# Performance work log

Measured on AMD Instinct MI355X. Metric: run time of the kernel, lower is better.

Reference implementation:

```python
import jax, jax.numpy as jnp
import numpy as np

N_NODES = 50000
N_EDGES = 640000
D_FEAT = 128
NUM_RELS = 8
EPS = 0.0  # init_eps=0, learn_eps=False -> constant buffer


def setup_inputs() -> dict:
    key = jax.random.key(0)
    k_feat, k_w, k_et, k_src, k_dst = jax.random.split(key, 5)
    feat = jax.random.normal(k_feat, (N_NODES, D_FEAT), dtype=jnp.float32)
    # TypedLinear weight: one [in_feat, out_feat] matrix per relation
    W = jax.random.normal(k_w, (NUM_RELS, D_FEAT, D_FEAT), dtype=jnp.float32) * 0.05
    etypes = jax.random.randint(k_et, (N_EDGES,), 0, NUM_RELS, dtype=jnp.int32)
    src = jax.random.randint(k_src, (N_EDGES,), 0, N_NODES, dtype=jnp.int32)
    dst = jax.random.randint(k_dst, (N_EDGES,), 0, N_NODES, dtype=jnp.int32)
    return {"feat": feat, "W": W, "etypes": etypes, "src": src, "dst": dst}


def reference(feat, W, etypes, src, dst):
    # feat: [N, d]; W: [R, d, d]; etypes/src/dst: [E]
    n_nodes = feat.shape[0]
    num_rels = W.shape[0]
    x = feat[src]  # gather source features, [E, d]
    # TypedLinear: m_e = x_e @ W[etype_e]. Loop over the small fixed relation
    # set (grouped-GEMM form) instead of materializing [E, d, d] weights.
    m = jnp.zeros_like(x)
    for r in range(num_rels):
        mask = (etypes == r)[:, None]
        m = m + jnp.where(mask, x, 0.0) @ W[r]
    # sum aggregation over destination nodes (update_all with fn.sum)
    neigh = jax.ops.segment_sum(m, dst, num_segments=n_nodes)  # [N, d]
    # GIN update: (1 + eps) * h + sum of messages; apply_func/activation are None
    return (1.0 + EPS) * feat + neigh
```

## Files before the change

kernel.cpp:

```cpp
#include <hip/hip_runtime.h>
#include <hip/hip_bf16.h>
#include <stdint.h>

#define D 128

using bf16x8 = __attribute__((ext_vector_type(8))) short;
using f32x4  = __attribute__((ext_vector_type(4))) float;

__device__ __forceinline__ unsigned short f2bf(float f) {
    unsigned u = __float_as_uint(f);
    u = (u + 0x7fffu + ((u >> 16) & 1u)) >> 16;
    return (unsigned short)u;
}
__device__ __forceinline__ float bf2f(unsigned short h) {
    return __uint_as_float(((unsigned)h) << 16);
}

__device__ __forceinline__ bf16x8 cvt8(float4 a, float4 b) {
    union { bf16x8 v; __hip_bfloat162 h[4]; } u;
    u.h[0] = __float22bfloat162_rn(make_float2(a.x, a.y));
    u.h[1] = __float22bfloat162_rn(make_float2(a.z, a.w));
    u.h[2] = __float22bfloat162_rn(make_float2(b.x, b.y));
    u.h[3] = __float22bfloat162_rn(make_float2(b.z, b.w));
    return u.v;
}

__device__ __forceinline__ uint4 pack2(f32x4 x, f32x4 y) {
    union { uint4 u; __hip_bfloat162 h[4]; } o;
    o.h[0] = __float22bfloat162_rn(make_float2(x[0], x[1]));
    o.h[1] = __float22bfloat162_rn(make_float2(x[2], x[3]));
    o.h[2] = __float22bfloat162_rn(make_float2(y[0], y[1]));
    o.h[3] = __float22bfloat162_rn(make_float2(y[2], y[3]));
    return o.u;
}

__global__ __launch_bounds__(256) void prep_wt_kernel(
    const float* __restrict__ W, unsigned short* __restrict__ Wt, int total)
{
    int idx = blockIdx.x * 256 + threadIdx.x;
    if (idx >= total) return;
    int r = idx >> 14;
    int rem = idx & 16383;
    int k = rem >> 7, c = rem & 127;
    Wt[(r << 14) + (c << 7) + k] = f2bf(W[idx]);
}

__global__ __launch_bounds__(256) void fused_transform_count_kernel(
    const float* __restrict__ feat, const unsigned short* __restrict__ Wt,
    unsigned short* __restrict__ H,
    const int* __restrict__ dst, int* __restrict__ deg, int* __restrict__ ord,
    int N, int NBX, int tBlocks, int E)
{
    __shared__ __align__(16) unsigned short sW[128 * 128];
    const int b = blockIdx.x;

    if (b >= tBlocks) {
        int e = (b - tBlocks) * 256 + threadIdx.x;
        if (e < E) ord[e] = atomicAdd(&deg[dst[e]], 1);
        return;
    }

    const int rel = b / NBX;
    const int bx  = b - rel * NBX;
    const int tid  = threadIdx.x;
    const int wave = tid >> 6, lane = tid & 63;
    const int q    = lane >> 4, mlo = lane & 15;

    {
        const ulonglong2* wsrc = (const ulonglong2*)(Wt + ((size_t)rel << 14));
        #pragma unroll
        for (int i = 0; i < 8; ++i) {
            int idx = tid + 256 * i;
            int row = idx >> 4, ch = idx & 15;
            ulonglong2 v = wsrc[idx];
            *(ulonglong2*)&sW[row * 128 + ((ch ^ (row & 15)) * 8)] = v;
        }
    }

    const int nb = bx * 128 + wave * 32;
    bf16x8 bfr[2][4];
    int nodeg[2];
    #pragma unroll
    for (int g = 0; g < 2; ++g) {
        int node = nb + g * 16 + mlo;
        nodeg[g] = node;
        int ld = node < N ? node : N - 1;
        const float* fp = feat + (size_t)ld * D + q * 8;
        #pragma unroll
        for (int ks = 0; ks < 4; ++ks)
            bfr[g][ks] = cvt8(*(const float4*)(fp + ks * 32), *(const float4*)(fp + ks * 32 + 4));
    }
    __syncthreads();

    const size_t Hb = (size_t)rel * N * D;
    unsigned short* hp0 = H + Hb + (size_t)nodeg[0] * D + q * 8;
    unsigned short* hp1 = H + Hb + (size_t)nodeg[1] * D + q * 8;

    #pragma unroll
    for (int j = 0; j < 4; ++j) {
        bf16x8 af0[4], af1[4];
        const int row0 = (2 * j) * 16 + mlo, row1 = row0 + 16;
        #pragma unroll
        for (int ks = 0; ks < 4; ++ks) {
            af0[ks] = *(const bf16x8*)&sW[row0 * 128 + (((ks * 4 + q) ^ mlo) * 8)];
            af1[ks] = *(const bf16x8*)&sW[row1 * 128 + (((ks * 4 + q) ^ mlo) * 8)];
        }
        #pragma unroll
        for (int g = 0; g < 2; ++g) {
            f32x4 a = {0.f,0.f,0.f,0.f}, c = {0.f,0.f,0.f,0.f};
            #pragma unroll
            for (int ks = 0; ks < 4; ++ks) {
                a = __builtin_amdgcn_mfma_f32_16x16x32_bf16(af0[ks], bfr[g][ks], a, 0, 0, 0);
                c = __builtin_amdgcn_mfma_f32_16x16x32_bf16(af1[ks], bfr[g][ks], c, 0, 0, 0);
            }
            if (nodeg[g] < N)
                *(uint4*)((g ? hp1 : hp0) + j * 32) = pack2(a, c);
        }
    }
}

__global__ __launch_bounds__(256) void k_blocksum(
    const int* __restrict__ deg, int* __restrict__ part, int N)
{
    int t = threadIdx.x, i = blockIdx.x * 256 + t;
    int v = (i < N) ? deg[i] : 0;
    #pragma unroll
    for (int o = 32; o > 0; o >>= 1) v += __shfl_down(v, o, 64);
    __shared__ int ws_[4];
    if ((t & 63) == 0) ws_[t >> 6] = v;
    __syncthreads();
    if (t == 0) part[blockIdx.x] = ws_[0] + ws_[1] + ws_[2] + ws_[3];
}

__global__ __launch_bounds__(256) void k_scanpart(int* part, int nb)
{
    __shared__ int s[256];
    int t = threadIdx.x;
    int v = (t < nb) ? part[t] : 0;
    s[t] = v;
    #pragma unroll
    for (int o = 1; o < 256; o <<= 1) {
        __syncthreads();
        int x = (t >= o) ? s[t - o] : 0;
        __syncthreads();
        s[t] += x;
    }
    if (t < nb) part[t] = s[t] - v;
}

__global__ __launch_bounds__(256) void k_scanfinal(
    const int* __restrict__ deg, const int* __restrict__ part,
    int* __restrict__ off, int N, int E)
{
    __shared__ int s[256];
    int t = threadIdx.x, i = blockIdx.x * 256 + t;
    int v = (i < N) ? deg[i] : 0;
    s[t] = v;
    #pragma unroll
    for (int o = 1; o < 256; o <<= 1) {
        __syncthreads();
        int x = (t >= o) ? s[t - o] : 0;
        __syncthreads();
        s[t] += x;
    }
    if (i < N) off[i] = part[blockIdx.x] + s[t] - v;
    if (i == 0) off[N] = E;
}

__global__ __launch_bounds__(256) void k_fill(
    const int* __restrict__ dst, const int* __restrict__ et,
    const int* __restrict__ src, const int* __restrict__ off,
    const int* __restrict__ ord, unsigned int* __restrict__ sorted, int E, int N)
{
    int e = blockIdx.x * 256 + threadIdx.x;
    if (e >= E) return;
    unsigned key = ((unsigned)et[e] * (unsigned)N + (unsigned)src[e]) << 8;
    sorted[off[dst[e]] + ord[e]] = key;
}

__global__ __launch_bounds__(256) void k_gather4(
    const char* __restrict__ Hc, const unsigned int* __restrict__ sorted,
    const int* __restrict__ off, const float* __restrict__ feat,
    float* __restrict__ out, int N)
{
    int n = blockIdx.x * 4 + (threadIdx.x >> 6);
    if (n >= N) return;
    int lane = threadIdx.x & 63;

    const int jj = lane >> 4, qq = (lane >> 2) & 3, pp = lane & 3;
    const int f = 16 * jj + 8 * (pp >> 1) + 2 * qq + (pp & 1);

    float2 acc = ((const float2*)feat)[(size_t)n * 64 + f];

    int j0 = __builtin_amdgcn_readfirstlane(off[n]);
    int j1 = __builtin_amdgcn_readfirstlane(off[n + 1]);
    int deg = j1 - j0;
    if (deg > 0) {
        unsigned ep = sorted[j0 + (lane < deg ? lane : deg - 1)];
        int capped = deg < 64 ? deg : 64;
        for (int done = 0; done < capped; done += 16) {
            unsigned a[16];
            #pragma unroll
            for (int u = 0; u < 16; ++u) {
                int idx = done + u; idx = idx < capped ? idx : capped - 1;
                unsigned p = __shfl(ep, idx);
                a[u] = *(const unsigned*)(Hc + p + lane * 4);
            }
            #pragma unroll
            for (int u = 0; u < 16; ++u) {
                bool v = (done + u) < capped;
                acc.x += v ? bf2f((unsigned short)(a[u] & 0xffffu)) : 0.f;
                acc.y += v ? bf2f((unsigned short)(a[u] >> 16)) : 0.f;
            }
        }
        for (int j = j0 + 64; j < j1; ++j) {
            unsigned p = sorted[j];
            unsigned a0 = *(const unsigned*)(Hc + p + lane * 4);
            acc.x += bf2f((unsigned short)(a0 & 0xffffu));
            acc.y += bf2f((unsigned short)(a0 >> 16));
        }
    }
    ((float2*)out)[(size_t)n * 64 + f] = acc;
}

__global__ __launch_bounds__(256) void init_kernel(
    const float* __restrict__ feat, float* __restrict__ out, int n4)
{
    int i = blockIdx.x * 256 + threadIdx.x;
    if (i < n4) ((float4*)out)[i] = ((const float4*)feat)[i];
}

__global__ __launch_bounds__(128) void edge_matvec_kernel(
    const float* __restrict__ feat, const float* __restrict__ W,
    const int* __restrict__ et, const int* __restrict__ src,
    const int* __restrict__ dst, float* __restrict__ out, int E)
{
    __shared__ float xs[D];
    int e = blockIdx.x;
    int c = threadIdx.x;
    int s = src[e], r = et[e], d = dst[e];
    xs[c] = feat[(size_t)s * D + c];
    __syncthreads();
    const float* Wr = W + (size_t)r * D * D;
    float acc = 0.f;
    #pragma unroll 8
    for (int k = 0; k < D; ++k) acc += xs[k] * Wr[(size_t)k * D + c];
    atomicAdd(out + (size_t)d * D + c, acc);
}

static inline size_t al256(size_t x) { return (x + 255) & ~(size_t)255; }

extern "C" void kernel_launch(void* const* d_in, const int* in_sizes, int n_in,
                              void* d_out, int out_size, void* d_ws, size_t ws_size,
                              hipStream_t stream) {
    const float* feat = (const float*)d_in[0];
    const float* W    = (const float*)d_in[1];
    const int*   et   = (const int*)d_in[2];
    const int*   src  = (const int*)d_in[3];
    const int*   dst  = (const int*)d_in[4];
    float* out = (float*)d_out;

    const int N = in_sizes[0] / D;
    const int R = in_sizes[1] / (D * D);
    const int E = in_sizes[2];

    size_t hB   = al256((size_t)R * N * D * sizeof(unsigned short));
    size_t wtB  = al256((size_t)R * D * D * sizeof(unsigned short));
    size_t offB = al256((size_t)(N + 1) * sizeof(int));
    size_t degB = al256((size_t)N * sizeof(int));
    size_t ordB = al256((size_t)E * sizeof(int));
    size_t parB = al256(1024 * sizeof(int));
    size_t srtB = al256((size_t)E * sizeof(unsigned int));
    size_t need = hB + wtB + offB + degB + ordB + parB + srtB;

    const int nbScan = (N + 255) / 256;
    const bool packable = (nbScan <= 256) &&
                          ((size_t)R * (size_t)N * 256ull <= 0xFFFFFFFFull);

    if (ws_size >= need && packable) {
        char* p = (char*)d_ws;
        unsigned short* H      = (unsigned short*)p;           p += hB;
        unsigned short* Wt     = (unsigned short*)p;           p += wtB;
        int*            off    = (int*)p;                      p += offB;
        int*            deg    = (int*)p;                      p += degB;
        int*            ord    = (int*)p;                      p += ordB;
        int*            part   = (int*)p;                      p += parB;
        unsigned int*   sorted = (unsigned int*)p;

        int wtTotal = R * D * D;
        int cntBlocks = (E + 255) / 256;

        hipMemsetAsync(deg, 0, (size_t)N * sizeof(int), stream);
        prep_wt_kernel<<<(wtTotal + 255) / 256, 256, 0, stream>>>(W, Wt, wtTotal);

        int NBX = (N + 127) / 128;
        int tBlocks = NBX * R;
        fused_transform_count_kernel<<<tBlocks + cntBlocks, 256, 0, stream>>>(
            feat, Wt, H, dst, deg, ord, N, NBX, tBlocks, E);

        k_blocksum<<<nbScan, 256, 0, stream>>>(deg, part, N);
        k_scanpart<<<1, 256, 0, stream>>>(part, nbScan);
        k_scanfinal<<<nbScan, 256, 0, stream>>>(deg, part, off, N, E);
        k_fill<<<cntBlocks, 256, 0, stream>>>(dst, et, src, off, ord, sorted, E, N);

        k_gather4<<<(N + 3) / 4, 256, 0, stream>>>((const char*)H, sorted, off, feat, out, N);
    } else {
        int n4 = (N * D) / 4;
        init_kernel<<<(n4 + 255) / 256, 256, 0, stream>>>(feat, out, n4);
        edge_matvec_kernel<<<E, 128, 0, stream>>>(feat, W, et, src, dst, out, E);
    }
}
```

Baseline: 201.8 us.

## Pre-convert features to bf16, interleave count blocks, widen gather loads

Adds a prep kernel that converts feat to bf16 once, so each of the 8 per-relation transform blocks reads half the bytes instead of re-reading fp32 features. Count blocks are spread evenly among transform blocks rather than appended at the end, so the atomic degree counting overlaps with the MFMA work. The gather kernel now has each half-wave handle a different edge with 8-byte loads and combines the halves with a cross-lane shuffle, which doubles the bytes per load instruction. This costs an extra bf16 feature buffer and an extra pass over feat.

```diff
diff --git a/kernel.cpp b/kernel.cpp
--- a/kernel.cpp
+++ b/kernel.cpp
@@ -34,34 +34,52 @@
     return o.u;
 }
 
-__global__ __launch_bounds__(256) void prep_wt_kernel(
-    const float* __restrict__ W, unsigned short* __restrict__ Wt, int total)
-{
-    int idx = blockIdx.x * 256 + threadIdx.x;
-    if (idx >= total) return;
-    int r = idx >> 14;
-    int rem = idx & 16383;
-    int k = rem >> 7, c = rem & 127;
-    Wt[(r << 14) + (c << 7) + k] = f2bf(W[idx]);
-}
-
-__global__ __launch_bounds__(256) void fused_transform_count_kernel(
-    const float* __restrict__ feat, const unsigned short* __restrict__ Wt,
+__global__ __launch_bounds__(256) void prep2_kernel(
+    const float* __restrict__ feat, unsigned short* __restrict__ featb,
+    const float* __restrict__ W, unsigned short* __restrict__ Wt,
+    int fcTotal , int wtTotal)
+{
+    int fcBlocks = (fcTotal + 255) >> 8;
+    int b = blockIdx.x;
+    if (b < fcBlocks) {
+        int i = b * 256 + threadIdx.x;
+        if (i < fcTotal) {
+            const float4* p = (const float4*)feat + (size_t)i * 2;
+            *(bf16x8*)(featb + (size_t)i * 8) = cvt8(p[0], p[1]);
+        }
+    } else {
+        int idx = (b - fcBlocks) * 256 + threadIdx.x;
+        if (idx < wtTotal) {
+            int r = idx >> 14;
+            int rem = idx & 16383;
+            int k = rem >> 7, c = rem & 127;
+            Wt[(r << 14) + (c << 7) + k] = f2bf(W[idx]);
+        }
+    }
+}
+
+__global__ __launch_bounds__(256) void fused2_kernel(
+    const unsigned short* __restrict__ featb, const unsigned short* __restrict__ Wt,
     unsigned short* __restrict__ H,
     const int* __restrict__ dst, int* __restrict__ deg, int* __restrict__ ord,
-    int N, int NBX, int tBlocks, int E)
+    int N, int NBX, int tBlocks, int cntBlocks, int E)
 {
     __shared__ __align__(16) unsigned short sW[128 * 128];
     const int b = blockIdx.x;
-
-    if (b >= tBlocks) {
-        int e = (b - tBlocks) * 256 + threadIdx.x;
+    const long long total = (long long)tBlocks + cntBlocks;
+
+    long long cb = ((long long)b * cntBlocks) / total;
+    bool isCount = (((long long)(b + 1) * cntBlocks) / total) > cb;
+
+    if (isCount) {
+        int e = (int)cb * 256 + threadIdx.x;
         if (e < E) ord[e] = atomicAdd(&deg[dst[e]], 1);
         return;
     }
 
-    const int rel = b / NBX;
-    const int bx  = b - rel * NBX;
+    const int tIdx = b - (int)cb;
+    const int rel = tIdx / NBX;
+    const int bx  = tIdx - rel * NBX;
     const int tid  = threadIdx.x;
     const int wave = tid >> 6, lane = tid & 63;
     const int q    = lane >> 4, mlo = lane & 15;
@@ -85,10 +103,10 @@
         int node = nb + g * 16 + mlo;
         nodeg[g] = node;
         int ld = node < N ? node : N - 1;
-        const float* fp = feat + (size_t)ld * D + q * 8;
+        const unsigned short* fp = featb + (size_t)ld * D + q * 8;
         #pragma unroll
         for (int ks = 0; ks < 4; ++ks)
-            bfr[g][ks] = cvt8(*(const float4*)(fp + ks * 32), *(const float4*)(fp + ks * 32 + 4));
+            bfr[g][ks] = *(const bf16x8*)(fp + ks * 32);
     }
     __syncthreads();
 
@@ -178,7 +196,7 @@
     sorted[off[dst[e]] + ord[e]] = key;
 }
 
-__global__ __launch_bounds__(256) void k_gather4(
+__global__ __launch_bounds__(256) void k_gather5(
     const char* __restrict__ Hc, const unsigned int* __restrict__ sorted,
     const int* __restrict__ off, const float* __restrict__ feat,
     float* __restrict__ out, int N)
@@ -186,41 +204,57 @@
     int n = blockIdx.x * 4 + (threadIdx.x >> 6);
     if (n >= N) return;
     int lane = threadIdx.x & 63;
-
-    const int jj = lane >> 4, qq = (lane >> 2) & 3, pp = lane & 3;
-    const int f = 16 * jj + 8 * (pp >> 1) + 2 * qq + (pp & 1);
-
-    float2 acc = ((const float2*)feat)[(size_t)n * 64 + f];
+    int h = lane >> 5, l5 = lane & 31;
+
+    float2 acc0 = {0.f, 0.f}, acc1 = {0.f, 0.f};
 
     int j0 = __builtin_amdgcn_readfirstlane(off[n]);
     int j1 = __builtin_amdgcn_readfirstlane(off[n + 1]);
     int deg = j1 - j0;
     if (deg > 0) {
+        int capped = deg < 64 ? deg : 64;
         unsigned ep = sorted[j0 + (lane < deg ? lane : deg - 1)];
-        int capped = deg < 64 ? deg : 64;
-        for (int done = 0; done < capped; done += 16) {
-            unsigned a[16];
+        for (int done = 0; done < capped; done += 32) {
+            unsigned long long a[16];
             #pragma unroll
             for (int u = 0; u < 16; ++u) {
-                int idx = done + u; idx = idx < capped ? idx : capped - 1;
-                unsigned p = __shfl(ep, idx);
-                a[u] = *(const unsigned*)(Hc + p + lane * 4);
+                int eidx = done + 2 * u + h;
+                int cl = eidx < capped ? eidx : capped - 1;
+                unsigned p = __shfl(ep, cl);
+                a[u] = *(const unsigned long long*)(Hc + p + l5 * 8);
             }
             #pragma unroll
             for (int u = 0; u < 16; ++u) {
-                bool v = (done + u) < capped;
-                acc.x += v ? bf2f((unsigned short)(a[u] & 0xffffu)) : 0.f;
-                acc.y += v ? bf2f((unsigned short)(a[u] >> 16)) : 0.f;
+                bool v = (done + 2 * u + h) < capped;
+                unsigned lo = (unsigned)a[u], hi = (unsigned)(a[u] >> 32);
+                acc0.x += v ? bf2f((unsigned short)(lo & 0xffffu)) : 0.f;
+                acc0.y += v ? bf2f((unsigned short)(lo >> 16)) : 0.f;
+                acc1.x += v ? bf2f((unsigned short)(hi & 0xffffu)) : 0.f;
+                acc1.y += v ? bf2f((unsigned short)(hi >> 16)) : 0.f;
             }
         }
-        for (int j = j0 + 64; j < j1; ++j) {
+        for (int j = j0 + 64 + h; j < j1; j += 2) {
             unsigned p = sorted[j];
-            unsigned a0 = *(const unsigned*)(Hc + p + lane * 4);
-            acc.x += bf2f((unsigned short)(a0 & 0xffffu));
-            acc.y += bf2f((unsigned short)(a0 >> 16));
-        }
-    }
-    ((float2*)out)[(size_t)n * 64 + f] = acc;
+            unsigned long long a0 = *(const unsigned long long*)(Hc + p + l5 * 8);
+            unsigned lo = (unsigned)a0, hi = (unsigned)(a0 >> 32);
+            acc0.x += bf2f((unsigned short)(lo & 0xffffu));
+            acc0.y += bf2f((unsigned short)(lo >> 16));
+            acc1.x += bf2f((unsigned short)(hi & 0xffffu));
+            acc1.y += bf2f((unsigned short)(hi >> 16));
+        }
+    }
+    acc0.x += __shfl(acc0.x, lane ^ 32);
+    acc0.y += __shfl(acc0.y, lane ^ 32);
+    acc1.x += __shfl(acc1.x, lane ^ 32);
+    acc1.y += __shfl(acc1.y, lane ^ 32);
+    if (h == 0) {
+        int f4 = 8 * (l5 >> 3) + 4 * (l5 & 1) + ((l5 >> 1) & 3);
+        float4 fv = ((const float4*)feat)[(size_t)n * 32 + f4];
+        float4 o;
+        o.x = fv.x + acc0.x; o.y = fv.y + acc0.y;
+        o.z = fv.z + acc1.x; o.w = fv.w + acc1.y;
+        ((float4*)out)[(size_t)n * 32 + f4] = o;
+    }
 }
 
 __global__ __launch_bounds__(256) void init_kernel(
@@ -271,7 +305,8 @@
     size_t ordB = al256((size_t)E * sizeof(int));
     size_t parB = al256(1024 * sizeof(int));
     size_t srtB = al256((size_t)E * sizeof(unsigned int));
-    size_t need = hB + wtB + offB + degB + ordB + parB + srtB;
+    size_t fbB  = al256((size_t)N * D * sizeof(unsigned short));
+    size_t need = hB + wtB + offB + degB + ordB + parB + srtB + fbB;
 
     const int nbScan = (N + 255) / 256;
     const bool packable = (nbScan <= 256) &&
@@ -285,25 +320,30 @@
         int*            deg    = (int*)p;                      p += degB;
         int*            ord    = (int*)p;                      p += ordB;
         int*            part   = (int*)p;                      p += parB;
-        unsigned int*   sorted = (unsigned int*)p;
+        unsigned int*   sorted = (unsigned int*)p;             p += srtB;
+        unsigned short* featb  = (unsigned short*)p;
 
         int wtTotal = R * D * D;
+        int fcTotal = (N * D) / 8;
+        int fcBlocks = (fcTotal + 255) / 256;
+        int wtBlocks = (wtTotal + 255) / 256;
         int cntBlocks = (E + 255) / 256;
 
         hipMemsetAsync(deg, 0, (size_t)N * sizeof(int), stream);
-        prep_wt_kernel<<<(wtTotal + 255) / 256, 256, 0, stream>>>(W, Wt, wtTotal);
+        prep2_kernel<<<fcBlocks + wtBlocks, 256, 0, stream>>>(
+            feat, featb, W, Wt, fcTotal, wtTotal);
 
         int NBX = (N + 127) / 128;
         int tBlocks = NBX * R;
-        fused_transform_count_kernel<<<tBlocks + cntBlocks, 256, 0, stream>>>(
-            feat, Wt, H, dst, deg, ord, N, NBX, tBlocks, E);
+        fused2_kernel<<<tBlocks + cntBlocks, 256, 0, stream>>>(
+            featb, Wt, H, dst, deg, ord, N, NBX, tBlocks, cntBlocks, E);
 
         k_blocksum<<<nbScan, 256, 0, stream>>>(deg, part, N);
         k_scanpart<<<1, 256, 0, stream>>>(part, nbScan);
         k_scanfinal<<<nbScan, 256, 0, stream>>>(deg, part, off, N, E);
         k_fill<<<cntBlocks, 256, 0, stream>>>(dst, et, src, off, ord, sorted, E, N);
 
-        k_gather4<<<(N + 3) / 4, 256, 0, stream>>>((const char*)H, sorted, off, feat, out, N);
+        k_gather5<<<(N + 3) / 4, 256, 0, stream>>>((const char*)H, sorted, off, feat, out, N);
     } else {
         int n4 = (N * D) / 4;
         init_kernel<<<(n4 + 255) / 256, 256, 0, stream>>>(feat, out, n4);
```

After: 178.9 us. -11.4%, faster.
